# Kernel optimization log

Measured on AMD Instinct MI355X. Metric: run time of the kernel, lower is better.

Reference implementation:

```python
import jax, jax.numpy as jnp
import numpy as np


def setup_inputs() -> dict:
    key = jax.random.key(0)
    k1, k2, k3, k4, k5, k6 = jax.random.split(key, 6)
    Ne, dim_in, dim_out, B, Nr, E = 100000, 128, 128, 4, 8, 200000
    return {
        "H": jax.random.normal(k1, (Ne, dim_in), dtype=jnp.float32),
        "A": jax.random.uniform(k2, (Nr, B), dtype=jnp.float32),
        "V": jax.random.uniform(k3, (B, dim_in, dim_out), dtype=jnp.float32),
        "edge_row": jax.random.randint(k4, (Nr, E), 0, Ne, dtype=jnp.int32),
        "edge_col": jax.random.randint(k5, (Nr, E), 0, Ne, dtype=jnp.int32),
        "edge_val": jax.random.uniform(k6, (Nr, E), dtype=jnp.float32),
    }


def reference(H, A, V, edge_row, edge_col, edge_val):
    # W = einsum('rb,bio->rio', A, V): basis-decomposed relation weights
    Ne = H.shape[0]
    Nr = A.shape[0]
    W = jnp.einsum('rb,bio->rio', A, V)            # [Nr, dim_in, dim_out]
    HxW = jnp.einsum('ni,rio->rno', H, W)          # [Nr, Ne, dim_out]
    # sparse T_r @ HxW_r: gather source rows (cols of T), scale by values,
    # scatter-add into destination rows. Done for all relations at once.
    msgs = HxW[jnp.arange(Nr)[:, None], edge_col] * edge_val[..., None]  # [Nr, E, dim_out]
    out = jax.ops.segment_sum(
        msgs.reshape(-1, msgs.shape[-1]),
        edge_row.reshape(-1),
        num_segments=Ne,
    )  # sum over relations folded into one segment_sum
    return out
```

## Files before the change

kernel.cpp:

```cpp
#include <hip/hip_runtime.h>

typedef __attribute__((ext_vector_type(8))) short short8;
typedef __attribute__((ext_vector_type(4))) float floatx4;

constexpr int DIM   = 128;
constexpr int NB    = 4;
constexpr int NR    = 8;
constexpr int BROWS = 512;
constexpr int BCAP  = 16384;

static __device__ __forceinline__ unsigned short f2bf(float f) {
    unsigned int u = __float_as_uint(f);
    u += 0x7FFFu + ((u >> 16) & 1u);
    return (unsigned short)(u >> 16);
}
static __device__ __forceinline__ float bf_lo(unsigned int h) {
    return __uint_as_float(h << 16);
}
static __device__ __forceinline__ float bf_hi(unsigned int h) {
    return __uint_as_float(h & 0xFFFF0000u);
}

__global__ __launch_bounds__(256) void build_vfrag(
    const float* __restrict__ V, unsigned short* __restrict__ VfragG)
{
    int idx  = blockIdx.x * 256 + threadIdx.x;
    int lane = idx & 63;
    int ks   = (idx >> 6) & 3;
    int ot   = (idx >> 8) & 7;
    int b    = idx >> 11;

    int o  = ot * 16 + (lane & 15);
    int kb = ks * 32 + (lane >> 4) * 8;

    short8 v;
#pragma unroll
    for (int j = 0; j < 8; ++j)
        v[j] = (short)f2bf(V[((size_t)b * DIM + kb + j) * DIM + o]);
    *reinterpret_cast<short8*>(VfragG + (size_t)idx * 8) = v;
}

__global__ __launch_bounds__(256) void build_wfrag(
    const float* __restrict__ A, const float* __restrict__ V,
    unsigned short* __restrict__ Wfrag)
{
    int idx  = blockIdx.x * 256 + threadIdx.x;
    int lane = idx & 63;
    int ks   = (idx >> 6) & 3;
    int ot   = (idx >> 8) & 7;
    int r    = idx >> 11;

    int o     = ot * 16 + (lane & 15);
    int kbase = ks * 32 + (lane >> 4) * 8;

    float a0 = A[r * NB + 0], a1 = A[r * NB + 1];
    float a2 = A[r * NB + 2], a3 = A[r * NB + 3];

    short8 v;
#pragma unroll
    for (int j = 0; j < 8; ++j) {
        int k = kbase + j;
        float w = a0 * V[(0 * DIM + k) * DIM + o]
                + a1 * V[(1 * DIM + k) * DIM + o]
                + a2 * V[(2 * DIM + k) * DIM + o]
                + a3 * V[(3 * DIM + k) * DIM + o];
        v[j] = (short)f2bf(w);
    }
    *reinterpret_cast<short8*>(Wfrag + (size_t)idx * 8) = v;
}

__global__ __launch_bounds__(256) void h_to_bf(
    const float* __restrict__ H, unsigned short* __restrict__ Hbf, int n8)
{
    int i = blockIdx.x * 256 + threadIdx.x;
    if (i >= n8) return;
    const float4* hp = reinterpret_cast<const float4*>(H) + (size_t)i * 2;
    float4 f0 = hp[0];
    float4 f1 = hp[1];
    short8 v;
    v[0] = (short)f2bf(f0.x); v[1] = (short)f2bf(f0.y);
    v[2] = (short)f2bf(f0.z); v[3] = (short)f2bf(f0.w);
    v[4] = (short)f2bf(f1.x); v[5] = (short)f2bf(f1.y);
    v[6] = (short)f2bf(f1.z); v[7] = (short)f2bf(f1.w);
    *reinterpret_cast<short8*>(Hbf + (size_t)i * 8) = v;
}

__global__ __launch_bounds__(256) void bucket_scatter(
    const int* __restrict__ erow, const int* __restrict__ ecol,
    const float* __restrict__ eval, int* __restrict__ bcnt,
    int2* __restrict__ sorted1, int n, int E, int chunk)
{
    __shared__ int cnt[256];
    __shared__ int base[256];
    int t = threadIdx.x;
    cnt[t] = 0;
    __syncthreads();

    int s = blockIdx.x * chunk;
    int e = s + chunk; if (e > n) e = n;

    for (int i = s + t; i < e; i += 256)
        atomicAdd(&cnt[erow[i] >> 9], 1);
    __syncthreads();

    int c = cnt[t];
    base[t] = (c > 0) ? atomicAdd(&bcnt[t], c) : 0;
    cnt[t] = 0;
    __syncthreads();

    for (int i = s + t; i < e; i += 256) {
        int row = erow[i];
        int bkt = row >> 9;
        int rank = atomicAdd(&cnt[bkt], 1);
        int r = (int)((unsigned)i / (unsigned)E);
        int2 m;
        m.x = ((row & (BROWS - 1)) << 20) | (r << 17) | ecol[i];
        m.y = __float_as_int(eval[i]);
        sorted1[(size_t)bkt * BCAP + base[bkt] + rank] = m;
    }
}

__global__ __launch_bounds__(256) void bucket_scan(
    const int* __restrict__ bcnt, int* __restrict__ bstart,
    int* __restrict__ rowStart, int nbuc, int Ne)
{
    __shared__ int sd[256];
    int t = threadIdx.x;
    int c = (t < nbuc) ? bcnt[t] : 0;
    sd[t] = c; __syncthreads();
#pragma unroll
    for (int off = 1; off < 256; off <<= 1) {
        int v = (t >= off) ? sd[t - off] : 0;
        __syncthreads();
        sd[t] += v;
        __syncthreads();
    }
    if (t < nbuc) bstart[t] = sd[t] - c;
    if (t == nbuc - 1) rowStart[Ne] = sd[t];
}

__global__ __launch_bounds__(256) void bucket_sort(
    const int2* __restrict__ sorted1, const int* __restrict__ bcnt,
    const int* __restrict__ bstart, int* __restrict__ rowStart,
    int2* __restrict__ sorted, int Ne)
{
    __shared__ int hcnt[BROWS];
    __shared__ int hoff[BROWS];
    int b = blockIdx.x;
    int t = threadIdx.x;
    hcnt[t] = 0; hcnt[t + 256] = 0;
    __syncthreads();

    int n = bcnt[b];
    const int2* src = sorted1 + (size_t)b * BCAP;

    for (int i = t; i < n; i += 256)
        atomicAdd(&hcnt[(unsigned)src[i].x >> 20], 1);
    __syncthreads();

    if (t == 0) {
        int run = 0;
#pragma unroll 8
        for (int j = 0; j < BROWS; ++j) { hoff[j] = run; run += hcnt[j]; }
    }
    __syncthreads();

    int bs = bstart[b];
    int rs = b * BROWS;
    int nr = Ne - rs; if (nr > BROWS) nr = BROWS;
    for (int j = t; j < nr; j += 256)
        rowStart[rs + j] = bs + hoff[j];

    hcnt[t] = 0; hcnt[t + 256] = 0;
    __syncthreads();

    for (int i = t; i < n; i += 256) {
        int2 m = src[i];
        int lr = (unsigned)m.x >> 20;
        int pos = bs + hoff[lr] + atomicAdd(&hcnt[lr], 1);
        sorted[pos] = m;
    }
}

__global__ __launch_bounds__(256) void agg_kernel(
    const unsigned short* __restrict__ Hbf,
    const int*  __restrict__ rowStart,
    const int2* __restrict__ sorted,
    const float* __restrict__ Aw,
    unsigned short* __restrict__ Agg, int Ne)
{
    int tid  = threadIdx.x;
    int wid  = __builtin_amdgcn_readfirstlane(blockIdx.x * 4 + (tid >> 6));
    if (wid >= Ne) return;
    int lane = tid & 63;

    int s = __builtin_amdgcn_readfirstlane(rowStart[wid]);
    int e = __builtin_amdgcn_readfirstlane(rowStart[wid + 1]);

    const float4* Af = reinterpret_cast<const float4*>(Aw);

    float2 acc[4];
#pragma unroll
    for (int b = 0; b < 4; ++b) { acc[b].x = 0.f; acc[b].y = 0.f; }

    int i = s;
    for (; i + 4 <= e; i += 4) {
        int2 m0 = sorted[i],     m1 = sorted[i + 1];
        int2 m2 = sorted[i + 2], m3 = sorted[i + 3];
        int k0 = __builtin_amdgcn_readfirstlane(m0.x);
        int k1 = __builtin_amdgcn_readfirstlane(m1.x);
        int k2 = __builtin_amdgcn_readfirstlane(m2.x);
        int k3 = __builtin_amdgcn_readfirstlane(m3.x);
        float v0 = __uint_as_float(__builtin_amdgcn_readfirstlane(m0.y));
        float v1 = __uint_as_float(__builtin_amdgcn_readfirstlane(m1.y));
        float v2 = __uint_as_float(__builtin_amdgcn_readfirstlane(m2.y));
        float v3 = __uint_as_float(__builtin_amdgcn_readfirstlane(m3.y));

        unsigned int h0 = reinterpret_cast<const unsigned int*>(
            Hbf + (size_t)(k0 & 0x1FFFF) * DIM)[lane];
        unsigned int h1 = reinterpret_cast<const unsigned int*>(
            Hbf + (size_t)(k1 & 0x1FFFF) * DIM)[lane];
        unsigned int h2 = reinterpret_cast<const unsigned int*>(
            Hbf + (size_t)(k2 & 0x1FFFF) * DIM)[lane];
        unsigned int h3 = reinterpret_cast<const unsigned int*>(
            Hbf + (size_t)(k3 & 0x1FFFF) * DIM)[lane];

        int kk[4] = {k0, k1, k2, k3};
        float vv[4] = {v0, v1, v2, v3};
        unsigned int hh[4] = {h0, h1, h2, h3};
#pragma unroll
        for (int u = 0; u < 4; ++u) {
            float4 a = Af[((unsigned)kk[u] >> 17) & 7];
            float hx = bf_lo(hh[u]), hy = bf_hi(hh[u]);
            float s0 = vv[u] * a.x, s1 = vv[u] * a.y;
            float s2 = vv[u] * a.z, s3 = vv[u] * a.w;
            acc[0].x += s0 * hx; acc[0].y += s0 * hy;
            acc[1].x += s1 * hx; acc[1].y += s1 * hy;
            acc[2].x += s2 * hx; acc[2].y += s2 * hy;
            acc[3].x += s3 * hx; acc[3].y += s3 * hy;
        }
    }
    for (; i < e; ++i) {
        int2 m = sorted[i];
        int k = __builtin_amdgcn_readfirstlane(m.x);
        float v = __uint_as_float(__builtin_amdgcn_readfirstlane(m.y));
        unsigned int h = reinterpret_cast<const unsigned int*>(
            Hbf + (size_t)(k & 0x1FFFF) * DIM)[lane];
        float4 a = Af[((unsigned)k >> 17) & 7];
        float hx = bf_lo(h), hy = bf_hi(h);
        float s0 = v * a.x, s1 = v * a.y, s2 = v * a.z, s3 = v * a.w;
        acc[0].x += s0 * hx; acc[0].y += s0 * hy;
        acc[1].x += s1 * hx; acc[1].y += s1 * hy;
        acc[2].x += s2 * hx; acc[2].y += s2 * hy;
        acc[3].x += s3 * hx; acc[3].y += s3 * hy;
    }

    unsigned short* arow = Agg + (size_t)wid * 512 + lane * 2;
#pragma unroll
    for (int b = 0; b < 4; ++b) {
        unsigned int pk = (unsigned int)f2bf(acc[b].x)
                        | ((unsigned int)f2bf(acc[b].y) << 16);
        *reinterpret_cast<unsigned int*>(arow + b * 128) = pk;
    }
}

__global__ __launch_bounds__(512) void vgemm_kernel(
    const unsigned short* __restrict__ Agg,
    const unsigned short* __restrict__ VfragG,
    float* __restrict__ out, int Ne, int nTiles)
{
    __shared__ short8 ldsV[4096];
    int half = blockIdx.x & 1;
    int blk  = blockIdx.x >> 1;
    int nblk = gridDim.x >> 1;
    int tid  = threadIdx.x;

    for (int i = tid; i < 4096; i += 512) {
        int lane = i & 63, ks = (i >> 6) & 3, otl = (i >> 8) & 3, b = i >> 10;
        int gi = ((b * 8 + half * 4 + otl) * 4 + ks) * 64 + lane;
        ldsV[i] = reinterpret_cast<const short8*>(VfragG)[gi];
    }
    __syncthreads();

    int wave = tid >> 6;
    int lane = tid & 63;
    int quad = lane >> 4, l15 = lane & 15;

    int wgid = blk * 8 + wave;
    int nw   = nblk * 8;

    for (int tile = wgid; tile < nTiles; tile += nw) {
        int node0 = tile * 16;
        int node  = node0 + l15;
        int rdnode = node < Ne ? node : Ne - 1;

        const short8* bp = reinterpret_cast<const short8*>(Agg)
                         + (size_t)rdnode * 64 + quad;
        short8 bf[16];
#pragma unroll
        for (int b = 0; b < 4; ++b)
#pragma unroll
            for (int ks = 0; ks < 4; ++ks)
                bf[b * 4 + ks] = bp[b * 16 + ks * 4];

        floatx4 acc[4];
#pragma unroll
        for (int o = 0; o < 4; ++o) acc[o] = (floatx4){0.f, 0.f, 0.f, 0.f};

#pragma unroll
        for (int b = 0; b < 4; ++b)
#pragma unroll
            for (int ks = 0; ks < 4; ++ks)
#pragma unroll
                for (int otl = 0; otl < 4; ++otl)
                    acc[otl] = __builtin_amdgcn_mfma_f32_16x16x32_bf16(
                        ldsV[((b * 4 + otl) * 4 + ks) * 64 + lane],
                        bf[b * 4 + ks], acc[otl], 0, 0, 0);

        if (node < Ne) {
            float* orow = out + (size_t)node * DIM + half * 64;
#pragma unroll
            for (int otl = 0; otl < 4; ++otl) {
                float4 st;
                st.x = acc[otl][0]; st.y = acc[otl][1];
                st.z = acc[otl][2]; st.w = acc[otl][3];
                *reinterpret_cast<float4*>(orow + otl * 16 + quad * 4) = st;
            }
        }
    }
}

__global__ __launch_bounds__(256) void rgcn_main(
    const unsigned short* __restrict__ Hbf,
    const unsigned short* __restrict__ Wfrag,
    const int*   __restrict__ erow,
    const int*   __restrict__ ecol,
    const float* __restrict__ eval,
    float*       __restrict__ out,
    int E, int groups_per_rel, int waves_per_rel)
{
    int wid  = blockIdx.x * 4 + (threadIdx.x >> 6);
    int lane = threadIdx.x & 63;
    int r    = wid & 7;
    int wr   = wid >> 3;
    int quad = lane >> 4;
    int l15  = lane & 15;

    short8 b[8][4];
    {
        const short8* wp = reinterpret_cast<const short8*>(
            Wfrag + (size_t)r * 16384);
#pragma unroll
        for (int ot = 0; ot < 8; ++ot)
#pragma unroll
            for (int ks = 0; ks < 4; ++ks)
                b[ot][ks] = wp[(ot * 4 + ks) * 64 + lane];
    }

    for (int g = wr; g < groups_per_rel; g += waves_per_rel) {
        int ebase = r * E + g * 16;
        int   colv = ecol[ebase + l15];
        int   rowv = erow[ebase + l15];
        float valv = eval[ebase + l15];

        short8 a[4];
        const unsigned short* hp = Hbf + (size_t)colv * DIM + quad * 8;
#pragma unroll
        for (int ks = 0; ks < 4; ++ks)
            a[ks] = *reinterpret_cast<const short8*>(hp + ks * 32);

        floatx4 acc[8];
#pragma unroll
        for (int ot = 0; ot < 8; ++ot) acc[ot] = (floatx4){0.f, 0.f, 0.f, 0.f};
#pragma unroll
        for (int ot = 0; ot < 8; ++ot)
#pragma unroll
            for (int ks = 0; ks < 4; ++ks)
                acc[ot] = __builtin_amdgcn_mfma_f32_16x16x32_bf16(
                    a[ks], b[ot][ks], acc[ot], 0, 0, 0);

        int   row4[4];
        float val4[4];
#pragma unroll
        for (int reg = 0; reg < 4; ++reg) {
            int src  = quad * 4 + reg;
            row4[reg] = __shfl(rowv, src, 64);
            val4[reg] = __shfl(valv, src, 64);
        }
#pragma unroll
        for (int ot = 0; ot < 8; ++ot)
#pragma unroll
            for (int reg = 0; reg < 4; ++reg) {
                float m = acc[ot][reg] * val4[reg];
                atomicAdd(out + (size_t)row4[reg] * DIM + ot * 16 + l15, m);
            }
    }
}

extern "C" void kernel_launch(void* const* d_in, const int* in_sizes, int n_in,
                              void* d_out, int out_size, void* d_ws, size_t ws_size,
                              hipStream_t stream)
{
    const float* H    = (const float*)d_in[0];
    const float* A    = (const float*)d_in[1];
    const float* V    = (const float*)d_in[2];
    const int*   erow = (const int*)d_in[3];
    const int*   ecol = (const int*)d_in[4];
    const float* eval = (const float*)d_in[5];
    float* out = (float*)d_out;

    int Ne    = in_sizes[0] / DIM;
    int NEtot = in_sizes[3];
    int E     = NEtot / NR;

    auto al = [](size_t x) { return (x + 255) & ~(size_t)255; };

    int nbuc = (Ne + BROWS - 1) / BROWS;

    size_t offHbf    = 0;
    size_t offVfrag  = offHbf    + al((size_t)Ne * DIM * 2);
    size_t offWfrag  = offVfrag  + al((size_t)8192 * 16);
    size_t offAgg    = offWfrag  + al((size_t)16384 * 16);
    size_t offRow    = offAgg    + al((size_t)Ne * 512 * 2);
    size_t offBcnt   = offRow    + al(((size_t)Ne + 2) * 4);
    size_t offBstart = offBcnt   + al((size_t)256 * 4);
    size_t offSort   = offBstart + al((size_t)256 * 4);
    size_t total     = offSort   + al((size_t)NEtot * 8);

    char* ws = (char*)d_ws;
    unsigned short* Hbf    = (unsigned short*)(ws + offHbf);
    unsigned short* VfragG = (unsigned short*)(ws + offVfrag);
    unsigned short* Wfrag  = (unsigned short*)(ws + offWfrag);

    int n8 = Ne * DIM / 8;
    h_to_bf<<<(n8 + 255) / 256, 256, 0, stream>>>(H, Hbf, n8);

    if (ws_size < total) {
        build_wfrag<<<64, 256, 0, stream>>>(A, V, Wfrag);
        hipMemsetAsync(d_out, 0, (size_t)Ne * DIM * sizeof(float), stream);
        int blocks = 4096;
        int waves_per_rel = blocks * 4 / NR;
        int groups_per_rel = E / 16;
        rgcn_main<<<blocks, 256, 0, stream>>>(Hbf, Wfrag, erow, ecol, eval, out,
                                              E, groups_per_rel, waves_per_rel);
        return;
    }

    unsigned short* Agg      = (unsigned short*)(ws + offAgg);
    int2*           sorted1  = (int2*)(ws + offAgg);
    int*            rowStart = (int*)(ws + offRow);
    int*            bcnt     = (int*)(ws + offBcnt);
    int*            bstart   = (int*)(ws + offBstart);
    int2*           sorted   = (int2*)(ws + offSort);

    build_vfrag<<<32, 256, 0, stream>>>(V, VfragG);

    hipMemsetAsync(bcnt, 0, 256 * 4, stream);
    int sblocks = 512;
    int chunk   = (NEtot + sblocks - 1) / sblocks;
    bucket_scatter<<<sblocks, 256, 0, stream>>>(erow, ecol, eval, bcnt,
                                                sorted1, NEtot, E, chunk);
    bucket_scan<<<1, 256, 0, stream>>>(bcnt, bstart, rowStart, nbuc, Ne);
    bucket_sort<<<nbuc, 256, 0, stream>>>(sorted1, bcnt, bstart, rowStart,
                                          sorted, Ne);

    agg_kernel<<<(Ne + 3) / 4, 256, 0, stream>>>(Hbf, rowStart, sorted, A,
                                                 Agg, Ne);

    int nTiles = (Ne + 15) / 16;
    vgemm_kernel<<<512, 512, 0, stream>>>(Agg, VfragG, out, Ne, nTiles);
}
```

Before: 332.7 us.

## Compute full output row per wave in vgemm and double-buffer Agg loads

The vgemm kernel now keeps all 128 output columns in one block, so LDS holds the full V fragment (128KB) and each Agg tile is read once rather than twice. Each wave double-buffers its register fragments, loading the next tile while running MFMAs on the current one. The first tile is fetched before the LDS fill to hide that latency. The grid is halved and launch bounds ask for two blocks per CU. The risks are higher register pressure (two 16-entry short8 buffers plus 8 accumulators) and LDS use that may limit occupancy.

```diff
diff --git a/kernel.cpp b/kernel.cpp
--- a/kernel.cpp
+++ b/kernel.cpp
@@ -264,68 +264,86 @@
     }
 }
 
-__global__ __launch_bounds__(512) void vgemm_kernel(
+__global__ __launch_bounds__(512, 2) void vgemm_kernel(
     const unsigned short* __restrict__ Agg,
     const unsigned short* __restrict__ VfragG,
     float* __restrict__ out, int Ne, int nTiles)
 {
-    __shared__ short8 ldsV[4096];
-    int half = blockIdx.x & 1;
-    int blk  = blockIdx.x >> 1;
-    int nblk = gridDim.x >> 1;
+    __shared__ short8 ldsV[8192];
     int tid  = threadIdx.x;
-
-    for (int i = tid; i < 4096; i += 512) {
-        int lane = i & 63, ks = (i >> 6) & 3, otl = (i >> 8) & 3, b = i >> 10;
-        int gi = ((b * 8 + half * 4 + otl) * 4 + ks) * 64 + lane;
-        ldsV[i] = reinterpret_cast<const short8*>(VfragG)[gi];
-    }
-    __syncthreads();
-
     int wave = tid >> 6;
     int lane = tid & 63;
     int quad = lane >> 4, l15 = lane & 15;
 
-    int wgid = blk * 8 + wave;
-    int nw   = nblk * 8;
-
-    for (int tile = wgid; tile < nTiles; tile += nw) {
-        int node0 = tile * 16;
-        int node  = node0 + l15;
+    int wgid = blockIdx.x * 8 + wave;
+    int nw   = gridDim.x * 8;
+
+    short8 bfA[16], bfB[16];
+
+    auto LOAD = [&](short8 (&bf)[16], int tile) {
+        int node = tile * 16 + l15;
         int rdnode = node < Ne ? node : Ne - 1;
-
         const short8* bp = reinterpret_cast<const short8*>(Agg)
                          + (size_t)rdnode * 64 + quad;
-        short8 bf[16];
 #pragma unroll
         for (int b = 0; b < 4; ++b)
 #pragma unroll
             for (int ks = 0; ks < 4; ++ks)
                 bf[b * 4 + ks] = bp[b * 16 + ks * 4];
-
-        floatx4 acc[4];
-#pragma unroll
-        for (int o = 0; o < 4; ++o) acc[o] = (floatx4){0.f, 0.f, 0.f, 0.f};
-
+    };
+
+    auto COMP = [&](const short8 (&bf)[16], int tile) {
+        floatx4 acc[8];
+#pragma unroll
+        for (int o = 0; o < 8; ++o) acc[o] = (floatx4){0.f, 0.f, 0.f, 0.f};
 #pragma unroll
         for (int b = 0; b < 4; ++b)
 #pragma unroll
             for (int ks = 0; ks < 4; ++ks)
 #pragma unroll
-                for (int otl = 0; otl < 4; ++otl)
-                    acc[otl] = __builtin_amdgcn_mfma_f32_16x16x32_bf16(
-                        ldsV[((b * 4 + otl) * 4 + ks) * 64 + lane],
-                        bf[b * 4 + ks], acc[otl], 0, 0, 0);
-
+                for (int ot = 0; ot < 8; ++ot)
+                    acc[ot] = __builtin_amdgcn_mfma_f32_16x16x32_bf16(
+                        ldsV[((b * 8 + ot) * 4 + ks) * 64 + lane],
+                        bf[b * 4 + ks], acc[ot], 0, 0, 0);
+        int node = tile * 16 + l15;
         if (node < Ne) {
-            float* orow = out + (size_t)node * DIM + half * 64;
-#pragma unroll
-            for (int otl = 0; otl < 4; ++otl) {
+            float* orow = out + (size_t)node * DIM;
+#pragma unroll
+            for (int ot = 0; ot < 8; ++ot) {
                 float4 st;
-                st.x = acc[otl][0]; st.y = acc[otl][1];
-                st.z = acc[otl][2]; st.w = acc[otl][3];
-                *reinterpret_cast<float4*>(orow + otl * 16 + quad * 4) = st;
+                st.x = acc[ot][0]; st.y = acc[ot][1];
+                st.z = acc[ot][2]; st.w = acc[ot][3];
+                *reinterpret_cast<float4*>(orow + ot * 16 + quad * 4) = st;
             }
+        }
+    };
+
+    int tile = wgid;
+    bool valid = tile < nTiles;
+    if (valid) LOAD(bfA, tile);
+
+    for (int i = tid; i < 8192; i += 512)
+        ldsV[i] = reinterpret_cast<const short8*>(VfragG)[i];
+    __syncthreads();
+
+    if (!valid) return;
+    for (;;) {
+        int t2 = tile + nw;
+        if (t2 < nTiles) {
+            LOAD(bfB, t2);
+            COMP(bfA, tile);
+            int t3 = t2 + nw;
+            if (t3 < nTiles) {
+                LOAD(bfA, t3);
+                COMP(bfB, t2);
+                tile = t3;
+            } else {
+                COMP(bfB, t2);
+                break;
+            }
+        } else {
+            COMP(bfA, tile);
+            break;
         }
     }
 }
@@ -468,5 +486,5 @@
                                                  Agg, Ne);
 
     int nTiles = (Ne + 15) / 16;
-    vgemm_kernel<<<512, 512, 0, stream>>>(Agg, VfragG, out, Ne, nTiles);
-}
+    vgemm_kernel<<<256, 512, 0, stream>>>(Agg, VfragG, out, Ne, nTiles);
+}
```

After: 495.5 us. 1.49x slower.
